# Kernel tuning notes

Hardware: AMD Instinct MI355X
Metric: run time of the kernel (lower is better)

Reference implementation:

```python
import jax, jax.numpy as jnp
import numpy as np

MODEL_DIM = 1024
HEAD_SIZE = 128

def setup_inputs() -> dict:
    key = jax.random.key(0)
    k0, k1, k2, k3 = jax.random.split(key, 4)
    embedded = jax.random.normal(k0, (4, 4096, MODEL_DIM), dtype=jnp.float32)
    # nn.Linear(model_dim, head_size, bias=False) weights: [head_size, model_dim]
    s = 1.0 / np.sqrt(MODEL_DIM)
    Wk = jax.random.uniform(k1, (HEAD_SIZE, MODEL_DIM), jnp.float32, -s, s)
    Wq = jax.random.uniform(k2, (HEAD_SIZE, MODEL_DIM), jnp.float32, -s, s)
    Wv = jax.random.uniform(k3, (HEAD_SIZE, MODEL_DIM), jnp.float32, -s, s)
    return {"embedded": embedded, "Wk": Wk, "Wq": Wq, "Wv": Wv}

def reference(embedded, Wk, Wq, Wv):
    # embedded: [b, s, m]; W*: [h, m]
    keys = jnp.einsum('bsm,hm->bsh', embedded, Wk)
    queries = jnp.einsum('bsm,hm->bsh', embedded, Wq)
    values = jnp.einsum('bsm,hm->bsh', embedded, Wv)
    h = keys.shape[-1]
    scores = jnp.einsum('bqh,bkh->bqk', queries, keys) / jnp.sqrt(jnp.float32(h))  # [b,s,s]
    s_len = keys.shape[1]
    causal = jnp.tril(jnp.ones((s_len, s_len), dtype=bool))
    scores = jnp.where(causal, scores, -jnp.inf)
    probs = jax.nn.softmax(scores, axis=-1)
    return jnp.einsum('bqk,bkh->bqh', probs, values)
```

## Files before the change

### kernel.cpp

```cpp
#include <hip/hip_runtime.h>
#include <hip/hip_bf16.h>


#define SEQ 4096
#define BATCH 4
#define HS 128
#define PSTRIDE ((size_t)BATCH * SEQ * HS)

typedef unsigned short u16;
typedef __bf16 bf16x8 __attribute__((ext_vector_type(8)));
typedef _Float16 f16x4 __attribute__((ext_vector_type(4)));
typedef float f32x4 __attribute__((ext_vector_type(4)));

__device__ __forceinline__ u16 f2bf(float f) {
    union { float f; unsigned u; } v; v.f = f;
    unsigned u = v.u;
    return (u16)((u + 0x7FFFu + ((u >> 16) & 1u)) >> 16);
}
__device__ __forceinline__ float bf2f(u16 u) {
    union { unsigned u; float f; } v; v.u = ((unsigned)u) << 16; return v.f;
}
__device__ __forceinline__ u16 f2h(float f) {
    union { _Float16 h; u16 u; } v; v.h = (_Float16)f; return v.u;
}
__device__ __forceinline__ void async_cp16(const void* g, void* l) {
    __builtin_amdgcn_global_load_lds(
        (const __attribute__((address_space(1))) unsigned int*)g,
        (__attribute__((address_space(3))) unsigned int*)l, 16, 0, 0);
}

__global__ __launch_bounds__(256) void wconv_kernel(
    const float* __restrict__ Wk, const float* __restrict__ Wq,
    const float* __restrict__ Wv, u16* __restrict__ Wt)
{
    const int g    = blockIdx.x * 256 + threadIdx.x;
    const int lane = g & 63;
    const int kf   = (g >> 6) & 1;
    const int kc   = (g >> 7) & 15;
    const int nt   = g >> 11;
    const int row  = nt * 16 + (lane & 15);
    const int k0   = kc * 64 + kf * 32 + (lane >> 4) * 8;
    const float* src = (row < 128) ? Wk : ((row < 256) ? Wq : Wv);
    const float scale = (row >= 128 && row < 256)
        ? 0.08838834764831845f * 1.4426950408889634f : 1.0f;
    const float4 v0 = *(const float4*)&src[(size_t)(row & 127) * 1024 + k0];
    const float4 v1 = *(const float4*)&src[(size_t)(row & 127) * 1024 + k0 + 4];
    ushort4 a, b;
    a.x = f2bf(v0.x * scale); a.y = f2bf(v0.y * scale);
    a.z = f2bf(v0.z * scale); a.w = f2bf(v0.w * scale);
    b.x = f2bf(v1.x * scale); b.y = f2bf(v1.y * scale);
    b.z = f2bf(v1.z * scale); b.w = f2bf(v1.w * scale);
    *(ushort4*)&Wt[(size_t)g * 8]     = a;
    *(ushort4*)&Wt[(size_t)g * 8 + 4] = b;
}

__global__ __launch_bounds__(256, 2) void qkv_kernel(
    const float* __restrict__ emb, const u16* __restrict__ Wt,
    u16* __restrict__ Qf, u16* __restrict__ Kf, u16* __restrict__ Vf)
{
    __shared__ u16 sE[2][32][72];
    __shared__ u16 sOut[32][392];

    const int tid  = threadIdx.x;
    const int wv   = tid >> 6;
    const int lane = tid & 63;
    const int quad = lane >> 4;
    const int l16  = lane & 15;
    const int R0   = blockIdx.x * 32;

    const int arow = tid >> 3, ac8 = tid & 7;
    const float* abase = &emb[(size_t)(R0 + arow) * 1024 + ac8 * 8];

    f32x4 acc[2][6];
    #pragma unroll
    for (int rg = 0; rg < 2; rg++)
        #pragma unroll
        for (int nt = 0; nt < 6; nt++) acc[rg][nt] = (f32x4){0.f, 0.f, 0.f, 0.f};

    bf16x8 B0[12], B1[12];

#define LOADB(kci, B)                                                          \
    {                                                                          \
        _Pragma("unroll")                                                      \
        for (int nt = 0; nt < 6; nt++) {                                       \
            const size_t g = ((size_t)((wv * 6 + nt) * 16 + (kci)) * 2) * 64 + lane; \
            B[2 * nt]     = *(const bf16x8*)&Wt[g * 8];                        \
            B[2 * nt + 1] = *(const bf16x8*)&Wt[(g + 64) * 8];                 \
        }                                                                      \
    }
#define WRITEA(buf, v0, v1)                                                    \
    {                                                                          \
        ushort4 lo, hi;                                                        \
        lo.x = f2bf((v0).x); lo.y = f2bf((v0).y);                              \
        lo.z = f2bf((v0).z); lo.w = f2bf((v0).w);                              \
        hi.x = f2bf((v1).x); hi.y = f2bf((v1).y);                              \
        hi.z = f2bf((v1).z); hi.w = f2bf((v1).w);                              \
        *(ushort4*)&sE[buf][arow][ac8 * 8]     = lo;                           \
        *(ushort4*)&sE[buf][arow][ac8 * 8 + 4] = hi;                           \
    }
#define COMPUTE(buf, B)                                                        \
    {                                                                          \
        bf16x8 a[2][2];                                                        \
        _Pragma("unroll")                                                      \
        for (int rg = 0; rg < 2; rg++)                                         \
            _Pragma("unroll")                                                  \
            for (int kf = 0; kf < 2; kf++)                                     \
                a[rg][kf] = *(const bf16x8*)&sE[buf][rg * 16 + l16][kf * 32 + quad * 8]; \
        _Pragma("unroll")                                                      \
        for (int nt = 0; nt < 6; nt++)                                         \
            _Pragma("unroll")                                                  \
            for (int rg = 0; rg < 2; rg++) {                                   \
                acc[rg][nt] = __builtin_amdgcn_mfma_f32_16x16x32_bf16(a[rg][0], B[2 * nt],     acc[rg][nt], 0, 0, 0); \
                acc[rg][nt] = __builtin_amdgcn_mfma_f32_16x16x32_bf16(a[rg][1], B[2 * nt + 1], acc[rg][nt], 0, 0, 0); \
            }                                                                  \
    }

    float4 av0 = *(const float4*)&abase[0];
    float4 av1 = *(const float4*)&abase[4];
    LOADB(0, B0);
    WRITEA(0, av0, av1);

    for (int it = 0; it < 8; it++) {
        const int k1 = 2 * it + 1;
        __syncthreads();
        av0 = *(const float4*)&abase[k1 * 64];
        av1 = *(const float4*)&abase[k1 * 64 + 4];
        LOADB(k1, B1);
        COMPUTE(0, B0);
        WRITEA(1, av0, av1);
        __syncthreads();
        if (it < 7) {
            av0 = *(const float4*)&abase[(k1 + 1) * 64];
            av1 = *(const float4*)&abase[(k1 + 1) * 64 + 4];
            LOADB(k1 + 1, B0);
        }
        COMPUTE(1, B1);
        if (it < 7) WRITEA(0, av0, av1);
    }

    #pragma unroll
    for (int nt = 0; nt < 6; nt++) {
        const int col = wv * 96 + nt * 16 + l16;
        #pragma unroll
        for (int rg = 0; rg < 2; rg++) {
            const int rl = rg * 16 + quad * 4;
            #pragma unroll
            for (int r = 0; r < 4; r++) {
                const float v = acc[rg][nt][r];
                sOut[rl + r][col] = (col < 256) ? f2bf(v) : f2h(v);
            }
        }
    }
    __syncthreads();

    const int b  = R0 >> 12;
    const int s0 = R0 & 4095;
    #pragma unroll
    for (int i = 0; i < 2; i++) {
        const int g    = tid + i * 256;
        const int lg   = g & 63;
        const int kfp  = (g >> 6) & 3;
        const int k16l = g >> 8;
        const int rl   = k16l * 16 + (lg & 15);
        const int cl   = kfp * 32 + (lg >> 4) * 8;
        const size_t base = (((size_t)(b * 256 + (s0 >> 4) + k16l) * 4 + kfp) * 64 + lg) * 8;
        *(uint4*)&Kf[base] = *(const uint4*)&sOut[rl][cl];
        *(uint4*)&Qf[base] = *(const uint4*)&sOut[rl][128 + cl];
    }
    #pragma unroll
    for (int i = 0; i < 4; i++) {
        const int g   = tid + i * 256;
        const int lg  = g & 63;
        const int ntl = (g >> 6) & 1;
        const int ht  = g >> 7;
        const int h   = ht * 16 + (lg & 15);
        const int kl  = ntl * 16 + ((lg >> 4) & 3) * 4;
        ushort4 o;
        o.x = sOut[kl + 0][256 + h];
        o.y = sOut[kl + 1][256 + h];
        o.z = sOut[kl + 2][256 + h];
        o.w = sOut[kl + 3][256 + h];
        const int t64 = s0 >> 6;
        const int ntg = ((s0 >> 4) & 3) + ntl;
        const size_t base = ((((size_t)(b * 64 + t64) * 8 + ht) * 4 + ntg) * 64 + lg) * 4;
        *(ushort4*)&Vf[base] = o;
    }
#undef LOADB
#undef WRITEA
#undef COMPUTE
}

template<int SPLIT>
__global__ __launch_bounds__(256, 2) void attn_kernel(
    const u16* __restrict__ Qf, const u16* __restrict__ Kf,
    const u16* __restrict__ Vf, u16* __restrict__ Opart,
    float* __restrict__ lpart, float* __restrict__ out)
{
    __shared__ u16 sT[2][16384];

    const int tid  = threadIdx.x;
    const int wv   = tid >> 6;
    const int lane = tid & 63;
    const int quad = lane >> 4;
    const int l16  = lane & 15;

    const int L = blockIdx.x;
    const int b = L & 3;
    const int u = L >> 2;
    int Q, sp;
    if constexpr (SPLIT == 1) {
        Q = u; sp = 0;
    } else {
        constexpr int half = SPLIT / 2;
        if (u < 32 * half) { Q = u / half; sp = u % half; }
        else { const int v = u - 32 * half; Q = 31 - v / half; sp = half + v % half; }
    }
    const int q0 = Q * 128;
    const int ktmax = 2 * Q + 1;
    const size_t bS = (size_t)b * SEQ;

    const char* KbB = (const char*)(Kf + (size_t)b * 524288);
    const char* VbB = (const char*)(Vf + (size_t)b * 524288);

    bf16x8 qf[2][4];
    #pragma unroll
    for (int qg = 0; qg < 2; qg++) {
        const int q16 = Q * 8 + wv * 2 + qg;
        #pragma unroll
        for (int kf = 0; kf < 4; kf++)
            qf[qg][kf] = *(const bf16x8*)&Qf[(((size_t)(b * 256 + q16) * 4 + kf) * 64 + lane) * 8];
    }

    float rs0 = 0.f, rs1 = 0.f;
    f32x4 O[2][8];
    #pragma unroll
    for (int qg = 0; qg < 2; qg++)
        #pragma unroll
        for (int ht = 0; ht < 8; ht++) O[qg][ht] = (f32x4){0.f, 0.f, 0.f, 0.f};

    const int qg0 = q0 + wv * 32 + l16;

    const int lseg = wv * 1024 + lane * 16;
#define STAGE(bufi, kt)                                                        \
    {                                                                          \
        const char* ks = KbB + (size_t)(kt) * 16384;                           \
        const char* vs = VbB + (size_t)(kt) * 16384;                           \
        char* lb = (char*)&sT[bufi][0] + wv * 1024;                            \
        _Pragma("unroll")                                                      \
        for (int i = 0; i < 4; i++)                                            \
            async_cp16(ks + i * 4096 + lseg, lb + i * 4096);                   \
        _Pragma("unroll")                                                      \
        for (int i = 0; i < 4; i++)                                            \
            async_cp16(vs + i * 4096 + lseg, lb + 16384 + i * 4096);           \
    }

    STAGE(0, sp);
    __syncthreads();

    int buf = 0;
    for (int kt = sp; kt <= ktmax; kt += SPLIT) {
        const int kb = kt * 64;
        if (kt + SPLIT <= ktmax) STAGE(buf ^ 1, kt + SPLIT);

        const bool diag = (kt >= 2 * Q);
        f16x4 pf0[4], pf1[4];
        #pragma unroll
        for (int nt = 0; nt < 4; nt++) {
            f32x4 s0 = (f32x4){0.f, 0.f, 0.f, 0.f};
            f32x4 s1 = (f32x4){0.f, 0.f, 0.f, 0.f};
            #pragma unroll
            for (int kf = 0; kf < 4; kf++) {
                const bf16x8 kfr = *(const bf16x8*)&sT[buf][((nt * 4 + kf) << 9) + lane * 8];
                s0 = __builtin_amdgcn_mfma_f32_16x16x32_bf16(kfr, qf[0][kf], s0, 0, 0, 0);
                s1 = __builtin_amdgcn_mfma_f32_16x16x32_bf16(kfr, qf[1][kf], s1, 0, 0, 0);
            }
            if (diag) {
                #pragma unroll
                for (int r = 0; r < 4; r++) {
                    const int kg = kb + nt * 16 + quad * 4 + r;
                    if (kg > qg0)      s0[r] = -3.0e38f;
                    if (kg > qg0 + 16) s1[r] = -3.0e38f;
                }
            }
            f16x4 p0, p1;
            #pragma unroll
            for (int r = 0; r < 4; r++) {
                const float e0 = exp2f(s0[r] - 4.0f);
                const float e1 = exp2f(s1[r] - 4.0f);
                rs0 += e0; rs1 += e1;
                p0[r] = (_Float16)e0; p1[r] = (_Float16)e1;
            }
            pf0[nt] = p0; pf1[nt] = p1;
        }

        #pragma unroll
        for (int ht = 0; ht < 8; ht++) {
            f16x4 vf[4];
            #pragma unroll
            for (int nt = 0; nt < 4; nt++)
                vf[nt] = *(const f16x4*)&sT[buf][8192 + ((ht * 4 + nt) << 8) + lane * 4];
            #pragma unroll
            for (int nt = 0; nt < 4; nt++) {
                O[0][ht] = __builtin_amdgcn_mfma_f32_16x16x16f16(vf[nt], pf0[nt], O[0][ht], 0, 0, 0);
                O[1][ht] = __builtin_amdgcn_mfma_f32_16x16x16f16(vf[nt], pf1[nt], O[1][ht], 0, 0, 0);
            }
        }

        __syncthreads();
        buf ^= 1;
    }
#undef STAGE

    rs0 += __shfl_xor(rs0, 16); rs0 += __shfl_xor(rs0, 32);
    rs1 += __shfl_xor(rs1, 16); rs1 += __shfl_xor(rs1, 32);

    if constexpr (SPLIT == 1) {
        #pragma unroll
        for (int qg = 0; qg < 2; qg++) {
            const float inv = 1.0f / (qg ? rs1 : rs0);
            const int q = q0 + wv * 32 + qg * 16 + l16;
            #pragma unroll
            for (int ht = 0; ht < 8; ht++) {
                f32x4 o = O[qg][ht] * inv;
                *(f32x4*)&out[(bS + q) * HS + ht * 16 + quad * 4] = o;
            }
        }
    } else {
        #pragma unroll
        for (int qg = 0; qg < 2; qg++)
            #pragma unroll
            for (int ht = 0; ht < 8; ht++) {
                const size_t j = ((size_t)((((b * 32 + Q) * 4 + wv) * 2 + qg) * 8 + ht)) * 64 + lane;
                ushort4 o;
                o.x = f2bf(O[qg][ht][0]); o.y = f2bf(O[qg][ht][1]);
                o.z = f2bf(O[qg][ht][2]); o.w = f2bf(O[qg][ht][3]);
                *(ushort4*)&Opart[(size_t)sp * PSTRIDE + j * 4] = o;
            }
        if (quad == 0) {
            lpart[((size_t)(sp * BATCH + b)) * SEQ + q0 + wv * 32 + l16]      = rs0;
            lpart[((size_t)(sp * BATCH + b)) * SEQ + q0 + wv * 32 + 16 + l16] = rs1;
        }
    }
}

template<int SPLIT>
__global__ __launch_bounds__(256) void merge_kernel(
    const u16* __restrict__ Opart, const float* __restrict__ lpart,
    float* __restrict__ out)
{
    const int g  = blockIdx.x * 256 + threadIdx.x;
    const int b  = g >> 17;
    const int q  = (g >> 5) & 4095;
    const int hc = g & 31;
    const int Qb = q >> 7, wvv = (q >> 5) & 3, qg = (q >> 4) & 1, l16 = q & 15;
    const int ht = hc >> 2, qd = hc & 3;
    const int lane = qd * 16 + l16;
    const size_t j4 = (((size_t)((((b * 32 + Qb) * 4 + wvv) * 2 + qg) * 8 + ht)) * 64 + lane) * 4;

    float den = 0.f;
    f32x4 num = (f32x4){0.f, 0.f, 0.f, 0.f};
    #pragma unroll
    for (int s = 0; s < SPLIT; s++) {
        den += lpart[((size_t)(s * BATCH + b)) * SEQ + q];
        const ushort4 o = *(const ushort4*)&Opart[(size_t)s * PSTRIDE + j4];
        num[0] += bf2f(o.x); num[1] += bf2f(o.y);
        num[2] += bf2f(o.z); num[3] += bf2f(o.w);
    }
    const float inv = 1.0f / den;
    float4 o; o.x = num[0] * inv; o.y = num[1] * inv;
    o.z = num[2] * inv; o.w = num[3] * inv;
    *(float4*)&out[(size_t)g * 4] = o;
}

extern "C" void kernel_launch(void* const* d_in, const int* in_sizes, int n_in,
                              void* d_out, int out_size, void* d_ws, size_t ws_size,
                              hipStream_t stream) {
    const float* emb = (const float*)d_in[0];
    const float* Wk  = (const float*)d_in[1];
    const float* Wq  = (const float*)d_in[2];
    const float* Wv  = (const float*)d_in[3];
    float* out = (float*)d_out;

    char* ws = (char*)d_ws;
    const size_t WBF_SZ    = (size_t)384 * 1024 * 2;
    const size_t QKV_SZ    = (size_t)BATCH * SEQ * HS * 2;
    const size_t Q_OFF     = WBF_SZ;
    const size_t K_OFF     = Q_OFF + QKV_SZ;
    const size_t V_OFF     = K_OFF + QKV_SZ;
    const size_t OPART_OFF = V_OFF + QKV_SZ;
    const size_t OPART_1   = PSTRIDE * 2;
    const size_t L_1       = (size_t)BATCH * SEQ * 4;

    u16* Wt = (u16*)ws;
    u16* Qf = (u16*)(ws + Q_OFF);
    u16* Kf = (u16*)(ws + K_OFF);
    u16* Vf = (u16*)(ws + V_OFF);

    wconv_kernel<<<dim3(192), dim3(256), 0, stream>>>(Wk, Wq, Wv, Wt);
    qkv_kernel<<<dim3(512), dim3(256), 0, stream>>>(emb, Wt, Qf, Kf, Vf);

    const size_t need4 = OPART_OFF + 4 * (OPART_1 + L_1);
    const size_t need2 = OPART_OFF + 2 * (OPART_1 + L_1);

    if (ws_size >= need4) {
        u16*   Opart = (u16*)(ws + OPART_OFF);
        float* lp    = (float*)(ws + OPART_OFF + 4 * OPART_1);
        attn_kernel<4><<<dim3(32 * BATCH * 4), dim3(256), 0, stream>>>(Qf, Kf, Vf, Opart, lp, out);
        merge_kernel<4><<<dim3(BATCH * SEQ * HS / 4 / 256), dim3(256), 0, stream>>>(Opart, lp, out);
    } else if (ws_size >= need2) {
        u16*   Opart = (u16*)(ws + OPART_OFF);
        float* lp    = (float*)(ws + OPART_OFF + 2 * OPART_1);
        attn_kernel<2><<<dim3(32 * BATCH * 2), dim3(256), 0, stream>>>(Qf, Kf, Vf, Opart, lp, out);
        merge_kernel<2><<<dim3(BATCH * SEQ * HS / 4 / 256), dim3(256), 0, stream>>>(Opart, lp, out);
    } else {
        attn_kernel<1><<<dim3(32 * BATCH), dim3(256), 0, stream>>>(Qf, Kf, Vf, nullptr, nullptr, out);
    }
}
```

Measured before the change: 166.3 us.

## Use variable per-row-block split-K with contiguous tiles and 512-thread attention blocks

Replaces the fixed strided split (2 or 4 splits per query block) with a per-query-block split count that grows with causal length. Each split now handles a contiguous range of key tiles, which is meant to balance work across 512 slots. Blocks grow to 512 threads (8 waves, 16 query rows each) so each wave holds half the accumulators. The aim is better load balance and occupancy, at the cost of a linear-scan slot lookup in both the attention and merge kernels, and fewer MFMAs per K/V LDS load.

```diff
diff --git a/kernel.cpp b/kernel.cpp
--- a/kernel.cpp
+++ b/kernel.cpp
@@ -5,7 +5,7 @@
 #define SEQ 4096
 #define BATCH 4
 #define HS 128
-#define PSTRIDE ((size_t)BATCH * SEQ * HS)
+#define SLOTS_PB 128
 
 typedef unsigned short u16;
 typedef __bf16 bf16x8 __attribute__((ext_vector_type(8)));
@@ -27,6 +27,9 @@
     __builtin_amdgcn_global_load_lds(
         (const __attribute__((address_space(1))) unsigned int*)g,
         (__attribute__((address_space(3))) unsigned int*)l, 16, 0, 0);
+}
+__device__ __forceinline__ int nsplit_of(int Q) {
+    return Q / 5 + 1 + (Q >= 23 ? 1 : 0);
 }
 
 __global__ __launch_bounds__(256) void wconv_kernel(
@@ -190,8 +193,8 @@
 #undef COMPUTE
 }
 
-template<int SPLIT>
-__global__ __launch_bounds__(256, 2) void attn_kernel(
+template<bool DIRECT>
+__global__ __launch_bounds__(512, 4) void attn_kernel(
     const u16* __restrict__ Qf, const u16* __restrict__ Kf,
     const u16* __restrict__ Vf, u16* __restrict__ Opart,
     float* __restrict__ lpart, float* __restrict__ out)
@@ -204,41 +207,45 @@
     const int quad = lane >> 4;
     const int l16  = lane & 15;
 
-    const int L = blockIdx.x;
-    const int b = L & 3;
-    const int u = L >> 2;
-    int Q, sp;
-    if constexpr (SPLIT == 1) {
-        Q = u; sp = 0;
+    const int L    = blockIdx.x;
+    const int b    = L & 3;
+    const int slot = L >> 2;
+
+    int Q = 0, sp = 0;
+    if constexpr (DIRECT) {
+        Q = slot; sp = 0;
     } else {
-        constexpr int half = SPLIT / 2;
-        if (u < 32 * half) { Q = u / half; sp = u % half; }
-        else { const int v = u - 32 * half; Q = 31 - v / half; sp = half + v % half; }
-    }
+        int acc = 0;
+        #pragma unroll 1
+        for (int qq = 0; qq < 32; ++qq) {
+            const int n = nsplit_of(qq);
+            if (slot < acc + n) { Q = qq; sp = slot - acc; break; }
+            acc += n;
+        }
+    }
+    const int total = 2 * Q + 2;
+    const int ns    = DIRECT ? 1 : nsplit_of(Q);
+    const int kbeg  = DIRECT ? 0 : (sp * total) / ns;
+    const int kend  = DIRECT ? total : ((sp + 1) * total) / ns;
+
     const int q0 = Q * 128;
-    const int ktmax = 2 * Q + 1;
     const size_t bS = (size_t)b * SEQ;
 
     const char* KbB = (const char*)(Kf + (size_t)b * 524288);
     const char* VbB = (const char*)(Vf + (size_t)b * 524288);
 
-    bf16x8 qf[2][4];
-    #pragma unroll
-    for (int qg = 0; qg < 2; qg++) {
-        const int q16 = Q * 8 + wv * 2 + qg;
-        #pragma unroll
-        for (int kf = 0; kf < 4; kf++)
-            qf[qg][kf] = *(const bf16x8*)&Qf[(((size_t)(b * 256 + q16) * 4 + kf) * 64 + lane) * 8];
-    }
-
-    float rs0 = 0.f, rs1 = 0.f;
-    f32x4 O[2][8];
-    #pragma unroll
-    for (int qg = 0; qg < 2; qg++)
-        #pragma unroll
-        for (int ht = 0; ht < 8; ht++) O[qg][ht] = (f32x4){0.f, 0.f, 0.f, 0.f};
-
-    const int qg0 = q0 + wv * 32 + l16;
+    bf16x8 qf[4];
+    const int q16 = Q * 8 + wv;
+    #pragma unroll
+    for (int kf = 0; kf < 4; kf++)
+        qf[kf] = *(const bf16x8*)&Qf[(((size_t)(b * 256 + q16) * 4 + kf) * 64 + lane) * 8];
+
+    float rs0 = 0.f;
+    f32x4 O[8];
+    #pragma unroll
+    for (int ht = 0; ht < 8; ht++) O[ht] = (f32x4){0.f, 0.f, 0.f, 0.f};
+
+    const int qg0 = q0 + wv * 16 + l16;
 
     const int lseg = wv * 1024 + lane * 16;
 #define STAGE(bufi, kt)                                                        \
@@ -247,50 +254,46 @@
         const char* vs = VbB + (size_t)(kt) * 16384;                           \
         char* lb = (char*)&sT[bufi][0] + wv * 1024;                            \
         _Pragma("unroll")                                                      \
-        for (int i = 0; i < 4; i++)                                            \
-            async_cp16(ks + i * 4096 + lseg, lb + i * 4096);                   \
+        for (int i = 0; i < 2; i++)                                            \
+            async_cp16(ks + i * 8192 + lseg, lb + i * 8192);                   \
         _Pragma("unroll")                                                      \
-        for (int i = 0; i < 4; i++)                                            \
-            async_cp16(vs + i * 4096 + lseg, lb + 16384 + i * 4096);           \
-    }
-
-    STAGE(0, sp);
+        for (int i = 0; i < 2; i++)                                            \
+            async_cp16(vs + i * 8192 + lseg, lb + 16384 + i * 8192);           \
+    }
+
+    STAGE(0, kbeg);
     __syncthreads();
 
     int buf = 0;
-    for (int kt = sp; kt <= ktmax; kt += SPLIT) {
+    for (int kt = kbeg; kt < kend; ++kt) {
         const int kb = kt * 64;
-        if (kt + SPLIT <= ktmax) STAGE(buf ^ 1, kt + SPLIT);
+        if (kt + 1 < kend) STAGE(buf ^ 1, kt + 1);
 
         const bool diag = (kt >= 2 * Q);
-        f16x4 pf0[4], pf1[4];
+        f16x4 pf0[4];
         #pragma unroll
         for (int nt = 0; nt < 4; nt++) {
             f32x4 s0 = (f32x4){0.f, 0.f, 0.f, 0.f};
-            f32x4 s1 = (f32x4){0.f, 0.f, 0.f, 0.f};
             #pragma unroll
             for (int kf = 0; kf < 4; kf++) {
                 const bf16x8 kfr = *(const bf16x8*)&sT[buf][((nt * 4 + kf) << 9) + lane * 8];
-                s0 = __builtin_amdgcn_mfma_f32_16x16x32_bf16(kfr, qf[0][kf], s0, 0, 0, 0);
-                s1 = __builtin_amdgcn_mfma_f32_16x16x32_bf16(kfr, qf[1][kf], s1, 0, 0, 0);
+                s0 = __builtin_amdgcn_mfma_f32_16x16x32_bf16(kfr, qf[kf], s0, 0, 0, 0);
             }
             if (diag) {
                 #pragma unroll
                 for (int r = 0; r < 4; r++) {
                     const int kg = kb + nt * 16 + quad * 4 + r;
-                    if (kg > qg0)      s0[r] = -3.0e38f;
-                    if (kg > qg0 + 16) s1[r] = -3.0e38f;
+                    if (kg > qg0) s0[r] = -3.0e38f;
                 }
             }
-            f16x4 p0, p1;
+            f16x4 p0;
             #pragma unroll
             for (int r = 0; r < 4; r++) {
                 const float e0 = exp2f(s0[r] - 4.0f);
-                const float e1 = exp2f(s1[r] - 4.0f);
-                rs0 += e0; rs1 += e1;
-                p0[r] = (_Float16)e0; p1[r] = (_Float16)e1;
+                rs0 += e0;
+                p0[r] = (_Float16)e0;
             }
-            pf0[nt] = p0; pf1[nt] = p1;
+            pf0[nt] = p0;
         }
 
         #pragma unroll
@@ -300,10 +303,8 @@
             for (int nt = 0; nt < 4; nt++)
                 vf[nt] = *(const f16x4*)&sT[buf][8192 + ((ht * 4 + nt) << 8) + lane * 4];
             #pragma unroll
-            for (int nt = 0; nt < 4; nt++) {
-                O[0][ht] = __builtin_amdgcn_mfma_f32_16x16x16f16(vf[nt], pf0[nt], O[0][ht], 0, 0, 0);
-                O[1][ht] = __builtin_amdgcn_mfma_f32_16x16x16f16(vf[nt], pf1[nt], O[1][ht], 0, 0, 0);
-            }
+            for (int nt = 0; nt < 4; nt++)
+                O[ht] = __builtin_amdgcn_mfma_f32_16x16x16f16(vf[nt], pf0[nt], O[ht], 0, 0, 0);
         }
 
         __syncthreads();
@@ -312,38 +313,30 @@
 #undef STAGE
 
     rs0 += __shfl_xor(rs0, 16); rs0 += __shfl_xor(rs0, 32);
-    rs1 += __shfl_xor(rs1, 16); rs1 += __shfl_xor(rs1, 32);
-
-    if constexpr (SPLIT == 1) {
-        #pragma unroll
-        for (int qg = 0; qg < 2; qg++) {
-            const float inv = 1.0f / (qg ? rs1 : rs0);
-            const int q = q0 + wv * 32 + qg * 16 + l16;
-            #pragma unroll
-            for (int ht = 0; ht < 8; ht++) {
-                f32x4 o = O[qg][ht] * inv;
-                *(f32x4*)&out[(bS + q) * HS + ht * 16 + quad * 4] = o;
-            }
+
+    if constexpr (DIRECT) {
+        const float inv = 1.0f / rs0;
+        const int q = q0 + wv * 16 + l16;
+        #pragma unroll
+        for (int ht = 0; ht < 8; ht++) {
+            f32x4 o = O[ht] * inv;
+            *(f32x4*)&out[(bS + q) * HS + ht * 16 + quad * 4] = o;
         }
     } else {
-        #pragma unroll
-        for (int qg = 0; qg < 2; qg++)
-            #pragma unroll
-            for (int ht = 0; ht < 8; ht++) {
-                const size_t j = ((size_t)((((b * 32 + Q) * 4 + wv) * 2 + qg) * 8 + ht)) * 64 + lane;
-                ushort4 o;
-                o.x = f2bf(O[qg][ht][0]); o.y = f2bf(O[qg][ht][1]);
-                o.z = f2bf(O[qg][ht][2]); o.w = f2bf(O[qg][ht][3]);
-                *(ushort4*)&Opart[(size_t)sp * PSTRIDE + j * 4] = o;
-            }
-        if (quad == 0) {
-            lpart[((size_t)(sp * BATCH + b)) * SEQ + q0 + wv * 32 + l16]      = rs0;
-            lpart[((size_t)(sp * BATCH + b)) * SEQ + q0 + wv * 32 + 16 + l16] = rs1;
-        }
-    }
-}
-
-template<int SPLIT>
+        const size_t slotbase = (size_t)b * SLOTS_PB + slot;
+        #pragma unroll
+        for (int ht = 0; ht < 8; ht++) {
+            const size_t j = ((slotbase * 8 + wv) * 8 + ht) * 64 + lane;
+            ushort4 o;
+            o.x = f2bf(O[ht][0]); o.y = f2bf(O[ht][1]);
+            o.z = f2bf(O[ht][2]); o.w = f2bf(O[ht][3]);
+            *(ushort4*)&Opart[j * 4] = o;
+        }
+        if (quad == 0)
+            lpart[slotbase * 128 + wv * 16 + l16] = rs0;
+    }
+}
+
 __global__ __launch_bounds__(256) void merge_kernel(
     const u16* __restrict__ Opart, const float* __restrict__ lpart,
     float* __restrict__ out)
@@ -352,17 +345,28 @@
     const int b  = g >> 17;
     const int q  = (g >> 5) & 4095;
     const int hc = g & 31;
-    const int Qb = q >> 7, wvv = (q >> 5) & 3, qg = (q >> 4) & 1, l16 = q & 15;
+    const int Q  = q >> 7;
+    const int ql = q & 127;
+    const int wvv = ql >> 4, l16 = q & 15;
     const int ht = hc >> 2, qd = hc & 3;
     const int lane = qd * 16 + l16;
-    const size_t j4 = (((size_t)((((b * 32 + Qb) * 4 + wvv) * 2 + qg) * 8 + ht)) * 64 + lane) * 4;
+
+    int pre = 0, ns = 0;
+    #pragma unroll 1
+    for (int qq = 0; qq < 32; ++qq) {
+        const int n = nsplit_of(qq);
+        if (qq < Q) pre += n;
+        else if (qq == Q) { ns = n; break; }
+    }
+    const size_t base_slot = (size_t)b * SLOTS_PB + pre;
 
     float den = 0.f;
     f32x4 num = (f32x4){0.f, 0.f, 0.f, 0.f};
-    #pragma unroll
-    for (int s = 0; s < SPLIT; s++) {
-        den += lpart[((size_t)(s * BATCH + b)) * SEQ + q];
-        const ushort4 o = *(const ushort4*)&Opart[(size_t)s * PSTRIDE + j4];
+    #pragma unroll 1
+    for (int s = 0; s < ns; s++) {
+        den += lpart[(base_slot + s) * 128 + ql];
+        const size_t j = (((base_slot + s) * 8 + wvv) * 8 + ht) * 64 + lane;
+        const ushort4 o = *(const ushort4*)&Opart[j * 4];
         num[0] += bf2f(o.x); num[1] += bf2f(o.y);
         num[2] += bf2f(o.z); num[3] += bf2f(o.w);
     }
@@ -388,8 +392,8 @@
     const size_t K_OFF     = Q_OFF + QKV_SZ;
     const size_t V_OFF     = K_OFF + QKV_SZ;
     const size_t OPART_OFF = V_OFF + QKV_SZ;
-    const size_t OPART_1   = PSTRIDE * 2;
-    const size_t L_1       = (size_t)BATCH * SEQ * 4;
+    const size_t OPART_SZ  = (size_t)BATCH * SLOTS_PB * 32768;
+    const size_t L_SZ      = (size_t)BATCH * SLOTS_PB * 128 * 4;
 
     u16* Wt = (u16*)ws;
     u16* Qf = (u16*)(ws + Q_OFF);
@@ -399,20 +403,14 @@
     wconv_kernel<<<dim3(192), dim3(256), 0, stream>>>(Wk, Wq, Wv, Wt);
     qkv_kernel<<<dim3(512), dim3(256), 0, stream>>>(emb, Wt, Qf, Kf, Vf);
 
-    const size_t need4 = OPART_OFF + 4 * (OPART_1 + L_1);
-    const size_t need2 = OPART_OFF + 2 * (OPART_1 + L_1);
-
-    if (ws_size >= need4) {
+    const size_t need = OPART_OFF + OPART_SZ + L_SZ;
+
+    if (ws_size >= need) {
         u16*   Opart = (u16*)(ws + OPART_OFF);
-        float* lp    = (float*)(ws + OPART_OFF + 4 * OPART_1);
-        attn_kernel<4><<<dim3(32 * BATCH * 4), dim3(256), 0, stream>>>(Qf, Kf, Vf, Opart, lp, out);
-        merge_kernel<4><<<dim3(BATCH * SEQ * HS / 4 / 256), dim3(256), 0, stream>>>(Opart, lp, out);
-    } else if (ws_size >= need2) {
-        u16*   Opart = (u16*)(ws + OPART_OFF);
-        float* lp    = (float*)(ws + OPART_OFF + 2 * OPART_1);
-        attn_kernel<2><<<dim3(32 * BATCH * 2), dim3(256), 0, stream>>>(Qf, Kf, Vf, Opart, lp, out);
-        merge_kernel<2><<<dim3(BATCH * SEQ * HS / 4 / 256), dim3(256), 0, stream>>>(Opart, lp, out);
+        float* lp    = (float*)(ws + OPART_OFF + OPART_SZ);
+        attn_kernel<false><<<dim3(4 * SLOTS_PB), dim3(512), 0, stream>>>(Qf, Kf, Vf, Opart, lp, out);
+        merge_kernel<<<dim3(BATCH * SEQ * HS / 4 / 256), dim3(256), 0, stream>>>(Opart, lp, out);
     } else {
-        attn_kernel<1><<<dim3(32 * BATCH), dim3(256), 0, stream>>>(Qf, Kf, Vf, nullptr, nullptr, out);
-    }
-}
+        attn_kernel<true><<<dim3(32 * BATCH), dim3(512), 0, stream>>>(Qf, Kf, Vf, nullptr, nullptr, out);
+    }
+}
```

Measured after the change: 159.2 us. 4.3% less time.
